# Kernel tuning notes

Measured on AMD Instinct MI355X. Metric: run time of the kernel, lower is better.

Reference implementation:

```python
import jax, jax.numpy as jnp
import numpy as np

HIDDEN = 1024
HEADS = 16
DK = HIDDEN // HEADS  # 64
B, N = 2, 2048


def setup_inputs() -> dict:
    key = jax.random.key(0)
    ks = jax.random.split(key, 12)
    s = 0.02
    return {
        "q": jax.random.normal(ks[0], (B, N, HIDDEN), jnp.float32),
        "k": jax.random.normal(ks[1], (B, N, HIDDEN), jnp.float32),
        "v": jax.random.normal(ks[2], (B, N, HIDDEN), jnp.float32),
        "attn_bias": jax.random.normal(ks[3], (B, N, N), jnp.float32),
        "attention_mask": jnp.zeros((B, N, N), jnp.float32),
        # projection weights stored [in, out]
        "Wq": jax.random.normal(ks[4], (HIDDEN, HIDDEN), jnp.float32) * s,
        "bq": jnp.zeros((HIDDEN,), jnp.float32),
        "Wk": jax.random.normal(ks[5], (HIDDEN, HIDDEN), jnp.float32) * s,
        "bk": jnp.zeros((HIDDEN,), jnp.float32),
        "Wv": jax.random.normal(ks[6], (HIDDEN, HIDDEN), jnp.float32) * s,
        "bv": jnp.zeros((HIDDEN,), jnp.float32),
        "Wo": jax.random.normal(ks[7], (HIDDEN, HIDDEN), jnp.float32) * s,
        "bo": jnp.zeros((HIDDEN,), jnp.float32),
    }


def reference(q, k, v, attn_bias, attention_mask, Wq, bq, Wk, bk, Wv, bv, Wo, bo):
    b, n, _ = q.shape
    scale = DK ** (-0.5)
    # project and split heads: [B, H, N, Dk]
    qh = (q @ Wq + bq).reshape(b, n, HEADS, DK).transpose(0, 2, 1, 3)
    kh = (k @ Wk + bk).reshape(b, -1, HEADS, DK).transpose(0, 2, 1, 3)
    vh = (v @ Wv + bv).reshape(b, -1, HEADS, DK).transpose(0, 2, 1, 3)
    # scaled scores + additive bias/mask broadcast over heads: [B, H, N, N]
    scores = jnp.einsum('bhnd,bhmd->bhnm', qh * scale, kh)
    scores = scores + attn_bias[:, None, :, :] + attention_mask[:, None, :, :]
    probs = jax.nn.softmax(scores, axis=-1)  # dropout is identity at inference
    ctx = jnp.einsum('bhnm,bhmd->bhnd', probs, vh)
    ctx = ctx.transpose(0, 2, 1, 3).reshape(b, n, HEADS * DK)
    return ctx @ Wo + bo
```

## Files before the change

kernel.cpp:

```cpp
#include <hip/hip_runtime.h>
#include <hip/hip_bf16.h>

#define HIDDEN 1024
#define NHEADS 16
#define DKH   64
#define BATCH 2
#define SEQ   2048
#define MTOT  (BATCH*SEQ)

using bf16x8 = __attribute__((ext_vector_type(8))) short;
using f32x4  = __attribute__((ext_vector_type(4))) float;
using u16x4  = __attribute__((ext_vector_type(4))) unsigned short;

__device__ __forceinline__ unsigned short f2bf(float f) {
    union { __hip_bfloat16 h; unsigned short u; } v;
    v.h = __float2bfloat16(f);
    return v.u;
}

__device__ __forceinline__ float asfloat(unsigned int u) {
    union { unsigned int u; float f; } v; v.u = u; return v.f;
}

__device__ __forceinline__ float fexp2(float x) {
#if __has_builtin(__builtin_amdgcn_exp2f)
    return __builtin_amdgcn_exp2f(x);
#else
    return exp2f(x);
#endif
}

__device__ __forceinline__ void gload16(const unsigned short* g, unsigned short* l) {
    __builtin_amdgcn_global_load_lds((const __attribute__((address_space(1))) void*)g,
                                     (__attribute__((address_space(3))) void*)l, 16, 0, 0);
}

#define L2E 1.44269504088896340736f

__global__ __launch_bounds__(256) void prep(const float4* __restrict__ q,
                                            const float4* __restrict__ k,
                                            const float4* __restrict__ v,
                                            u16x4* __restrict__ qkv_bf,
                                            const float* __restrict__ Wq,
                                            const float* __restrict__ Wk,
                                            const float* __restrict__ Wv,
                                            const float* __restrict__ Wo,
                                            unsigned short* __restrict__ wt,
                                            const float* __restrict__ bias,
                                            const float* __restrict__ mask,
                                            unsigned short* __restrict__ biasf) {
    __shared__ __align__(16) char sh[16640];
    float (*tile)[65] = (float (*)[65])sh;
    unsigned short (*lb)[520] = (unsigned short (*)[520])sh;
    const int bid = blockIdx.x, t = threadIdx.x;
    if (bid < 12288) {
        int i = bid * 256 + t;
        const int per = MTOT * HIDDEN / 4;
        const float4* src; int tt;
        if (i < per)            { src = q; tt = 0; }
        else if (i < 2 * per)   { src = k; tt = 1; }
        else                    { src = v; tt = 2; }
        float4 f = src[i - tt * per];
        u16x4 o; o.x = f2bf(f.x); o.y = f2bf(f.y); o.z = f2bf(f.z); o.w = f2bf(f.w);
        qkv_bf[i] = o;
    } else if (bid < 13312) {
        int r = bid - 12288;
        const int z = r >> 8; r &= 255;
        const int kb = (r >> 4) * 64, nb = (r & 15) * 64;
        const float* W = (z == 0) ? Wq : (z == 1) ? Wk : (z == 2) ? Wv : Wo;
        unsigned short* out = wt + (size_t)z * HIDDEN * HIDDEN;
        #pragma unroll
        for (int i = 0; i < 16; i++) {
            int idx = i * 256 + t; int rr = idx >> 6, c = idx & 63;
            tile[rr][c] = W[(size_t)(kb + rr) * HIDDEN + nb + c];
        }
        __syncthreads();
        #pragma unroll
        for (int i = 0; i < 16; i++) {
            int idx = i * 256 + t; int n = idx >> 6, kk = idx & 63;
            out[(size_t)(nb + n) * HIDDEN + kb + kk] = f2bf(tile[kk][n]);
        }
    } else {
        const int cb = bid - 13312;
        const int chunk = cb & 3, g = (cb >> 2) & 127, b = cb >> 9;
        const float* bp = bias + ((size_t)b * SEQ + g * 16) * SEQ + chunk * 512;
        const float* mp = mask + ((size_t)b * SEQ + g * 16) * SEQ + chunk * 512;
        #pragma unroll
        for (int i = 0; i < 8; i++) {
            int idx = i * 256 + t;
            int row = idx >> 7, c4 = (idx & 127) * 4;
            float4 bv4 = *(const float4*)(bp + (size_t)row * SEQ + c4);
            float4 mv4 = *(const float4*)(mp + (size_t)row * SEQ + c4);
            union { u16x4 v; unsigned short s[4]; } o;
            o.s[0] = f2bf((bv4.x + mv4.x) * L2E);
            o.s[1] = f2bf((bv4.y + mv4.y) * L2E);
            o.s[2] = f2bf((bv4.z + mv4.z) * L2E);
            o.s[3] = f2bf((bv4.w + mv4.w) * L2E);
            *(u16x4*)&lb[row][c4] = o.v;
        }
        __syncthreads();
        const int w = t >> 6, ln = t & 63;
        const int quad = ln >> 4, c16 = ln & 15;
        unsigned short* ob = biasf + (((size_t)b * 128 + g) * 64 + chunk * 16) * 512 + ln * 8;
        #pragma unroll
        for (int it = 0; it < 4; it++) {
            int ttl = it * 4 + w;
            *(bf16x8*)(ob + (size_t)ttl * 512) = *(const bf16x8*)&lb[c16][ttl * 32 + quad * 8];
        }
    }
}

__device__ __forceinline__ void gemm_core_128(const unsigned short* __restrict__ X,
                                              const unsigned short* __restrict__ Wt,
                                              unsigned short* smem,
                                              int mbase, int nbase, f32x4 acc[4][4]) {
    const int tid = threadIdx.x, w = tid >> 6, ln = tid & 63;
    const int qr = (w >> 1) * 64, qc = (w & 1) * 64;
    const int g = ln >> 4, c16 = ln & 15;
    #pragma unroll
    for (int rt = 0; rt < 4; rt++)
        #pragma unroll
        for (int ct = 0; ct < 4; ct++) acc[rt][ct] = (f32x4){0.f, 0.f, 0.f, 0.f};

    for (int kk = 0; kk < HIDDEN; kk += 64) {
        __syncthreads();
        #pragma unroll
        for (int pass = 0; pass < 4; pass++) {
            int L = pass * 256 + tid;
            int r = L >> 3, c = (L & 7) ^ (r & 7);
            gload16(X  + (size_t)(mbase + r) * HIDDEN + kk + c * 8,
                    smem + (size_t)(pass * 256 + w * 64) * 8);
            gload16(Wt + (size_t)(nbase + r) * HIDDEN + kk + c * 8,
                    smem + 8192 + (size_t)(pass * 256 + w * 64) * 8);
        }
        __syncthreads();
        #pragma unroll
        for (int ks = 0; ks < 2; ks++) {
            bf16x8 af[4], bfr[4];
            #pragma unroll
            for (int rt = 0; rt < 4; rt++) {
                int r = qr + rt * 16 + c16;
                int ch = (g + ks * 4) ^ (r & 7);
                af[rt] = *(const bf16x8*)(smem + (size_t)(r * 8 + ch) * 8);
            }
            #pragma unroll
            for (int ct = 0; ct < 4; ct++) {
                int n = qc + ct * 16 + c16;
                int ch = (g + ks * 4) ^ (n & 7);
                bfr[ct] = *(const bf16x8*)(smem + 8192 + (size_t)(n * 8 + ch) * 8);
            }
            #pragma unroll
            for (int rt = 0; rt < 4; rt++)
                #pragma unroll
                for (int ct = 0; ct < 4; ct++)
                    acc[rt][ct] = __builtin_amdgcn_mfma_f32_16x16x32_bf16(af[rt], bfr[ct], acc[rt][ct], 0, 0, 0);
        }
    }
    __syncthreads();
}

__global__ __launch_bounds__(256, 2) void proj_gemm(const unsigned short* __restrict__ Xall,
                                                    const unsigned short* __restrict__ Wtall,
                                                    const float* __restrict__ bq,
                                                    const float* __restrict__ bk,
                                                    const float* __restrict__ bv,
                                                    unsigned short* __restrict__ qh,
                                                    unsigned short* __restrict__ khs,
                                                    unsigned short* __restrict__ vts) {
    __shared__ __align__(16) unsigned short smem[18432];
    const int z = blockIdx.z;
    const unsigned short* X  = Xall  + (size_t)z * MTOT * HIDDEN;
    const unsigned short* Wt = Wtall + (size_t)z * HIDDEN * HIDDEN;
    const float* bias = (z == 0) ? bq : (z == 1) ? bk : bv;
    const int mbase = blockIdx.x * 128, nbase = blockIdx.y * 128;
    const int tid = threadIdx.x, w = tid >> 6, ln = tid & 63;
    const int qr = (w >> 1) * 64, qc = (w & 1) * 64;
    const int g = ln >> 4, c16 = ln & 15;

    f32x4 acc[4][4];
    gemm_core_128(X, Wt, smem, mbase, nbase, acc);

    const float scale = (z == 0) ? (0.125f * L2E) : 1.0f;
    float bias_v[4];
    #pragma unroll
    for (int ct = 0; ct < 4; ct++) bias_v[ct] = bias[nbase + qc + ct * 16 + c16];

    unsigned short* eld = smem + w * 4608;
    #pragma unroll
    for (int rt = 0; rt < 4; rt++)
        #pragma unroll
        for (int ct = 0; ct < 4; ct++)
            #pragma unroll
            for (int r4 = 0; r4 < 4; r4++) {
                int row_l = rt * 16 + g * 4 + r4;
                int col_l = ct * 16 + c16;
                float val = (acc[rt][ct][r4] + bias_v[ct]) * scale;
                if (z == 2) eld[col_l * 72 + row_l] = f2bf(val);
                else        eld[row_l * 72 + col_l] = f2bf(val);
            }
    __syncthreads();

    const int b = mbase >> 11;
    const int pos0 = (mbase & 2047) + qr;
    const int h = (nbase + qc) >> 6;
    const int bh = b * NHEADS + h;
    if (z == 0) {
        const int row8 = ln >> 3, col8 = (ln & 7) * 8;
        unsigned short* dst0 = qh + ((size_t)bh * SEQ + pos0) * DKH;
        #pragma unroll
        for (int j = 0; j < 8; j++) {
            int row = j * 8 + row8;
            *(bf16x8*)(dst0 + row * 64 + col8) = *(const bf16x8*)&eld[row * 72 + col8];
        }
    } else if (z == 1) {
        unsigned short* base = khs + ((size_t)bh * 64 + (pos0 >> 5)) * 2048;
        const int kvp = (c16 >> 2) * 8 + (c16 & 3);
        #pragma unroll
        for (int j = 0; j < 8; j++) {
            int tloc = j >> 2, ks = (j >> 1) & 1, kvs = j & 1;
            int kvl = tloc * 32 + kvp + kvs * 4;
            *(bf16x8*)(base + tloc * 2048 + ks * 1024 + kvs * 512 + ln * 8)
                = *(const bf16x8*)&eld[kvl * 72 + ks * 32 + g * 8];
        }
    } else {
        unsigned short* base = vts + ((size_t)bh * 64 + (pos0 >> 5)) * 2048;
        #pragma unroll
        for (int j = 0; j < 8; j++) {
            int tloc = j >> 2, dt = j & 3;
            *(bf16x8*)(base + tloc * 2048 + dt * 512 + ln * 8)
                = *(const bf16x8*)&eld[(dt * 16 + c16) * 72 + tloc * 32 + g * 8];
        }
    }
}

__global__ __launch_bounds__(256, 2) void attn(const unsigned short* __restrict__ qh,
                                               const unsigned short* __restrict__ khs,
                                               const unsigned short* __restrict__ vts,
                                               const unsigned short* __restrict__ biasf,
                                               unsigned short* __restrict__ ctx) {
    __shared__ __align__(16) unsigned short smem[16384];
    const int tid = threadIdx.x, w = tid >> 6, ln = tid & 63;
    const int quad = ln >> 4, c16 = ln & 15;
    const int bid = blockIdx.x;
    const int xcd = bid & 7, jj = bid >> 3;
    const int bh = xcd * 4 + (jj >> 4);
    const int qb = jj & 15;
    const int b = bh >> 4, h = bh & 15;

    bf16x8 qf[2][2];
    #pragma unroll
    for (int qsub = 0; qsub < 2; qsub++) {
        const unsigned short* qp = qh + ((size_t)bh * SEQ + qb * 128 + w * 32 + qsub * 16 + c16) * DKH + quad * 8;
        qf[qsub][0] = *(const bf16x8*)qp;
        qf[qsub][1] = *(const bf16x8*)(qp + 32);
    }

    const unsigned short* kT = khs + (size_t)bh * 131072;
    const unsigned short* vT = vts + (size_t)bh * 131072;
    const unsigned short* bb0 = biasf + (((size_t)b * 128 + qb * 8 + w * 2) * 64) * 512 + ln * 8;
    const unsigned short* bb1 = bb0 + 32768;

    f32x4 accv[4][2];
    #pragma unroll
    for (int dt = 0; dt < 4; dt++)
        #pragma unroll
        for (int qsub = 0; qsub < 2; qsub++) accv[dt][qsub] = (f32x4){0.f, 0.f, 0.f, 0.f};
    float lacc[2] = {0.f, 0.f};

    bf16x8 bcur[2][4];
    #pragma unroll
    for (int j = 0; j < 4; j++) {
        bcur[0][j] = *(const bf16x8*)(bb0 + j * 512);
        bcur[1][j] = *(const bf16x8*)(bb1 + j * 512);
    }

    for (int T = 0; T < 16; T++) {
        __syncthreads();
        {
            const unsigned short* ksrc = kT + T * 8192 + w * 512 + ln * 8;
            const unsigned short* vsrc = vT + T * 8192 + w * 512 + ln * 8;
            unsigned short* lk = smem + w * 512;
            unsigned short* lv = smem + 8192 + w * 512;
            #pragma unroll
            for (int p = 0; p < 4; p++) {
                gload16(ksrc + p * 2048, lk + p * 2048);
                gload16(vsrc + p * 2048, lv + p * 2048);
            }
        }
        bf16x8 bnext[2][4];
        {
            const int Tn = (T < 15) ? T + 1 : 15;
            #pragma unroll
            for (int j = 0; j < 4; j++) {
                bnext[0][j] = *(const bf16x8*)(bb0 + (Tn * 4 + j) * 512);
                bnext[1][j] = *(const bf16x8*)(bb1 + (Tn * 4 + j) * 512);
            }
        }
        __syncthreads();
        #pragma unroll
        for (int j = 0; j < 4; j++) {
            bf16x8 kf00 = *(const bf16x8*)(smem + j * 2048 + ln * 8);
            bf16x8 kf01 = *(const bf16x8*)(smem + j * 2048 + 512 + ln * 8);
            bf16x8 kf10 = *(const bf16x8*)(smem + j * 2048 + 1024 + ln * 8);
            bf16x8 kf11 = *(const bf16x8*)(smem + j * 2048 + 1536 + ln * 8);
            bf16x8 vf[4];
            #pragma unroll
            for (int dt = 0; dt < 4; dt++)
                vf[dt] = *(const bf16x8*)(smem + 8192 + j * 2048 + dt * 512 + ln * 8);
            #pragma unroll
            for (int qsub = 0; qsub < 2; qsub++) {
                const unsigned int* bd = (const unsigned int*)&bcur[qsub][j];
                f32x4 s0, s1;
                s0[0] = asfloat(bd[0] << 16); s0[1] = asfloat(bd[0] & 0xFFFF0000u);
                s0[2] = asfloat(bd[1] << 16); s0[3] = asfloat(bd[1] & 0xFFFF0000u);
                s1[0] = asfloat(bd[2] << 16); s1[1] = asfloat(bd[2] & 0xFFFF0000u);
                s1[2] = asfloat(bd[3] << 16); s1[3] = asfloat(bd[3] & 0xFFFF0000u);
                s0 = __builtin_amdgcn_mfma_f32_16x16x32_bf16(kf00, qf[qsub][0], s0, 0, 0, 0);
                s0 = __builtin_amdgcn_mfma_f32_16x16x32_bf16(kf10, qf[qsub][1], s0, 0, 0, 0);
                s1 = __builtin_amdgcn_mfma_f32_16x16x32_bf16(kf01, qf[qsub][0], s1, 0, 0, 0);
                s1 = __builtin_amdgcn_mfma_f32_16x16x32_bf16(kf11, qf[qsub][1], s1, 0, 0, 0);
                #pragma unroll
                for (int r = 0; r < 4; r++) { s0[r] = fexp2(s0[r]); s1[r] = fexp2(s1[r]); }
                lacc[qsub] += ((s0[0] + s0[1]) + (s0[2] + s0[3]))
                            + ((s1[0] + s1[1]) + (s1[2] + s1[3]));
                union { bf16x8 v; __hip_bfloat162 hh[4]; } pu;
                pu.hh[0] = __float22bfloat162_rn(make_float2(s0[0], s0[1]));
                pu.hh[1] = __float22bfloat162_rn(make_float2(s0[2], s0[3]));
                pu.hh[2] = __float22bfloat162_rn(make_float2(s1[0], s1[1]));
                pu.hh[3] = __float22bfloat162_rn(make_float2(s1[2], s1[3]));
                #pragma unroll
                for (int dt = 0; dt < 4; dt++)
                    accv[dt][qsub] = __builtin_amdgcn_mfma_f32_16x16x32_bf16(vf[dt], pu.v, accv[dt][qsub], 0, 0, 0);
            }
            bcur[0][j] = bnext[0][j];
            bcur[1][j] = bnext[1][j];
        }
    }

    float inv[2];
    #pragma unroll
    for (int qsub = 0; qsub < 2; qsub++) {
        float l = lacc[qsub];
        l += __shfl_xor(l, 16);
        l += __shfl_xor(l, 32);
        inv[qsub] = 1.0f / l;
    }
    __syncthreads();
    unsigned short* ot = smem + w * 2304;
    #pragma unroll
    for (int dt = 0; dt < 4; dt++)
        #pragma unroll
        for (int qsub = 0; qsub < 2; qsub++)
            #pragma unroll
            for (int r = 0; r < 4; r += 2) {
                union { __hip_bfloat162 hh; unsigned int u; } pk;
                pk.hh = __float22bfloat162_rn(make_float2(accv[dt][qsub][r] * inv[qsub],
                                                         accv[dt][qsub][r + 1] * inv[qsub]));
                *(unsigned int*)&ot[(qsub * 16 + c16) * 72 + dt * 16 + quad * 4 + r] = pk.u;
            }
    const int qrow2 = ln >> 1, half = ln & 1;
    const unsigned short* srcp = ot + qrow2 * 72 + half * 32;
    unsigned short* dstp = ctx + ((size_t)b * SEQ + qb * 128 + w * 32 + qrow2) * HIDDEN
                         + h * 64 + half * 32;
    #pragma unroll
    for (int kk = 0; kk < 4; kk++)
        *(bf16x8*)(dstp + kk * 8) = *(const bf16x8*)(srcp + kk * 8);
}

__global__ __launch_bounds__(256, 2) void outproj(const unsigned short* __restrict__ X,
                                                  const unsigned short* __restrict__ Wt,
                                                  const float* __restrict__ bo,
                                                  float* __restrict__ out) {
    __shared__ __align__(16) unsigned short smem[16384];
    const int mbase = blockIdx.x * 128, nbase = blockIdx.y * 128;
    const int tid = threadIdx.x, w = tid >> 6, ln = tid & 63;
    const int qr = (w >> 1) * 64, qc = (w & 1) * 64;
    const int g = ln >> 4, c16 = ln & 15;

    f32x4 acc[4][4];
    gemm_core_128(X, Wt, smem, mbase, nbase, acc);

    float bo_v[4];
    #pragma unroll
    for (int ct = 0; ct < 4; ct++) bo_v[ct] = bo[nbase + qc + ct * 16 + c16];
    #pragma unroll
    for (int rt = 0; rt < 4; rt++)
        #pragma unroll
        for (int ct = 0; ct < 4; ct++)
            #pragma unroll
            for (int r4 = 0; r4 < 4; r4++)
                out[(size_t)(mbase + qr + rt * 16 + g * 4 + r4) * HIDDEN + nbase + qc + ct * 16 + c16]
                    = acc[rt][ct][r4] + bo_v[ct];
}

extern "C" void kernel_launch(void* const* d_in, const int* in_sizes, int n_in,
                              void* d_out, int out_size, void* d_ws, size_t ws_size,
                              hipStream_t stream) {
    const float* q    = (const float*)d_in[0];
    const float* k    = (const float*)d_in[1];
    const float* v    = (const float*)d_in[2];
    const float* bias = (const float*)d_in[3];
    const float* mask = (const float*)d_in[4];
    const float* Wq   = (const float*)d_in[5];
    const float* bq   = (const float*)d_in[6];
    const float* Wk   = (const float*)d_in[7];
    const float* bk   = (const float*)d_in[8];
    const float* Wv   = (const float*)d_in[9];
    const float* bv   = (const float*)d_in[10];
    const float* Wo   = (const float*)d_in[11];
    const float* bo   = (const float*)d_in[12];

    char* ws = (char*)d_ws;
    unsigned short* qkv_bf = (unsigned short*)(ws);
    unsigned short* wt     = (unsigned short*)(ws + 25165824);
    unsigned short* qh     = (unsigned short*)(ws + 33554432);
    unsigned short* khs    = (unsigned short*)(ws + 41943040);
    unsigned short* vts    = (unsigned short*)(ws + 50331648);
    unsigned short* ctx    = (unsigned short*)(ws + 58720256);
    unsigned short* biasf  = (unsigned short*)(ws + 67108864);

    prep<<<14336, 256, 0, stream>>>((const float4*)q, (const float4*)k, (const float4*)v,
                                    (u16x4*)qkv_bf, Wq, Wk, Wv, Wo, wt, bias, mask, biasf);
    proj_gemm<<<dim3(32, 8, 3), 256, 0, stream>>>(qkv_bf, wt, bq, bk, bv, qh, khs, vts);
    attn<<<512, 256, 0, stream>>>(qh, khs, vts, biasf, ctx);
    outproj<<<dim3(32, 8), 256, 0, stream>>>(ctx, wt + (size_t)3 * HIDDEN * HIDDEN, bo,
                                             (float*)d_out);
}
```

Before: 270.3 us.

## Halve attention query tile to 64 rows and double block count

Each attention block now handles 64 query rows instead of 128, with every wave covering 16 rows instead of 32. The grid grows from 512 to 1024 blocks and launch bounds allow four blocks per CU, so register use per thread drops and more waves are resident to hide latency. In exchange, every K/V tile staged in LDS is reused by half as many queries, which doubles the global and LDS traffic for K and V.

New measurement: 280.1 us. 3.6% more time.

```diff
diff --git a/kernel.cpp b/kernel.cpp
--- a/kernel.cpp
+++ b/kernel.cpp
@@ -233,7 +233,7 @@
     }
 }
 
-__global__ __launch_bounds__(256, 2) void attn(const unsigned short* __restrict__ qh,
+__global__ __launch_bounds__(256, 4) void attn(const unsigned short* __restrict__ qh,
                                                const unsigned short* __restrict__ khs,
                                                const unsigned short* __restrict__ vts,
                                                const unsigned short* __restrict__ biasf,
@@ -243,36 +243,29 @@
     const int quad = ln >> 4, c16 = ln & 15;
     const int bid = blockIdx.x;
     const int xcd = bid & 7, jj = bid >> 3;
-    const int bh = xcd * 4 + (jj >> 4);
-    const int qb = jj & 15;
+    const int bh = xcd * 4 + (jj >> 5);
+    const int qb = jj & 31;
     const int b = bh >> 4, h = bh & 15;
 
-    bf16x8 qf[2][2];
-    #pragma unroll
-    for (int qsub = 0; qsub < 2; qsub++) {
-        const unsigned short* qp = qh + ((size_t)bh * SEQ + qb * 128 + w * 32 + qsub * 16 + c16) * DKH + quad * 8;
-        qf[qsub][0] = *(const bf16x8*)qp;
-        qf[qsub][1] = *(const bf16x8*)(qp + 32);
+    bf16x8 qf[2];
+    {
+        const unsigned short* qp = qh + ((size_t)bh * SEQ + qb * 64 + w * 16 + c16) * DKH + quad * 8;
+        qf[0] = *(const bf16x8*)qp;
+        qf[1] = *(const bf16x8*)(qp + 32);
     }
 
     const unsigned short* kT = khs + (size_t)bh * 131072;
     const unsigned short* vT = vts + (size_t)bh * 131072;
-    const unsigned short* bb0 = biasf + (((size_t)b * 128 + qb * 8 + w * 2) * 64) * 512 + ln * 8;
-    const unsigned short* bb1 = bb0 + 32768;
-
-    f32x4 accv[4][2];
-    #pragma unroll
-    for (int dt = 0; dt < 4; dt++)
-        #pragma unroll
-        for (int qsub = 0; qsub < 2; qsub++) accv[dt][qsub] = (f32x4){0.f, 0.f, 0.f, 0.f};
-    float lacc[2] = {0.f, 0.f};
-
-    bf16x8 bcur[2][4];
-    #pragma unroll
-    for (int j = 0; j < 4; j++) {
-        bcur[0][j] = *(const bf16x8*)(bb0 + j * 512);
-        bcur[1][j] = *(const bf16x8*)(bb1 + j * 512);
-    }
+    const unsigned short* bb = biasf + (((size_t)b * 128 + qb * 4 + w) * 64) * 512 + ln * 8;
+
+    f32x4 accv[4];
+    #pragma unroll
+    for (int dt = 0; dt < 4; dt++) accv[dt] = (f32x4){0.f, 0.f, 0.f, 0.f};
+    float lacc = 0.f;
+
+    bf16x8 bcur[4];
+    #pragma unroll
+    for (int j = 0; j < 4; j++) bcur[j] = *(const bf16x8*)(bb + j * 512);
 
     for (int T = 0; T < 16; T++) {
         __syncthreads();
@@ -287,14 +280,12 @@
                 gload16(vsrc + p * 2048, lv + p * 2048);
             }
         }
-        bf16x8 bnext[2][4];
+        bf16x8 bnext[4];
         {
             const int Tn = (T < 15) ? T + 1 : 15;
             #pragma unroll
-            for (int j = 0; j < 4; j++) {
-                bnext[0][j] = *(const bf16x8*)(bb0 + (Tn * 4 + j) * 512);
-                bnext[1][j] = *(const bf16x8*)(bb1 + (Tn * 4 + j) * 512);
-            }
+            for (int j = 0; j < 4; j++)
+                bnext[j] = *(const bf16x8*)(bb + (Tn * 4 + j) * 512);
         }
         __syncthreads();
         #pragma unroll
@@ -307,64 +298,53 @@
             #pragma unroll
             for (int dt = 0; dt < 4; dt++)
                 vf[dt] = *(const bf16x8*)(smem + 8192 + j * 2048 + dt * 512 + ln * 8);
-            #pragma unroll
-            for (int qsub = 0; qsub < 2; qsub++) {
-                const unsigned int* bd = (const unsigned int*)&bcur[qsub][j];
-                f32x4 s0, s1;
-                s0[0] = asfloat(bd[0] << 16); s0[1] = asfloat(bd[0] & 0xFFFF0000u);
-                s0[2] = asfloat(bd[1] << 16); s0[3] = asfloat(bd[1] & 0xFFFF0000u);
-                s1[0] = asfloat(bd[2] << 16); s1[1] = asfloat(bd[2] & 0xFFFF0000u);
-                s1[2] = asfloat(bd[3] << 16); s1[3] = asfloat(bd[3] & 0xFFFF0000u);
-                s0 = __builtin_amdgcn_mfma_f32_16x16x32_bf16(kf00, qf[qsub][0], s0, 0, 0, 0);
-                s0 = __builtin_amdgcn_mfma_f32_16x16x32_bf16(kf10, qf[qsub][1], s0, 0, 0, 0);
-                s1 = __builtin_amdgcn_mfma_f32_16x16x32_bf16(kf01, qf[qsub][0], s1, 0, 0, 0);
-                s1 = __builtin_amdgcn_mfma_f32_16x16x32_bf16(kf11, qf[qsub][1], s1, 0, 0, 0);
-                #pragma unroll
-                for (int r = 0; r < 4; r++) { s0[r] = fexp2(s0[r]); s1[r] = fexp2(s1[r]); }
-                lacc[qsub] += ((s0[0] + s0[1]) + (s0[2] + s0[3]))
-                            + ((s1[0] + s1[1]) + (s1[2] + s1[3]));
-                union { bf16x8 v; __hip_bfloat162 hh[4]; } pu;
-                pu.hh[0] = __float22bfloat162_rn(make_float2(s0[0], s0[1]));
-                pu.hh[1] = __float22bfloat162_rn(make_float2(s0[2], s0[3]));
-                pu.hh[2] = __float22bfloat162_rn(make_float2(s1[0], s1[1]));
-                pu.hh[3] = __float22bfloat162_rn(make_float2(s1[2], s1[3]));
-                #pragma unroll
-                for (int dt = 0; dt < 4; dt++)
-                    accv[dt][qsub] = __builtin_amdgcn_mfma_f32_16x16x32_bf16(vf[dt], pu.v, accv[dt][qsub], 0, 0, 0);
-            }
-            bcur[0][j] = bnext[0][j];
-            bcur[1][j] = bnext[1][j];
+            const unsigned int* bd = (const unsigned int*)&bcur[j];
+            f32x4 s0, s1;
+            s0[0] = asfloat(bd[0] << 16); s0[1] = asfloat(bd[0] & 0xFFFF0000u);
+            s0[2] = asfloat(bd[1] << 16); s0[3] = asfloat(bd[1] & 0xFFFF0000u);
+            s1[0] = asfloat(bd[2] << 16); s1[1] = asfloat(bd[2] & 0xFFFF0000u);
+            s1[2] = asfloat(bd[3] << 16); s1[3] = asfloat(bd[3] & 0xFFFF0000u);
+            s0 = __builtin_amdgcn_mfma_f32_16x16x32_bf16(kf00, qf[0], s0, 0, 0, 0);
+            s0 = __builtin_amdgcn_mfma_f32_16x16x32_bf16(kf10, qf[1], s0, 0, 0, 0);
+            s1 = __builtin_amdgcn_mfma_f32_16x16x32_bf16(kf01, qf[0], s1, 0, 0, 0);
+            s1 = __builtin_amdgcn_mfma_f32_16x16x32_bf16(kf11, qf[1], s1, 0, 0, 0);
+            #pragma unroll
+            for (int r = 0; r < 4; r++) { s0[r] = fexp2(s0[r]); s1[r] = fexp2(s1[r]); }
+            lacc += ((s0[0] + s0[1]) + (s0[2] + s0[3]))
+                  + ((s1[0] + s1[1]) + (s1[2] + s1[3]));
+            union { bf16x8 v; __hip_bfloat162 hh[4]; } pu;
+            pu.hh[0] = __float22bfloat162_rn(make_float2(s0[0], s0[1]));
+            pu.hh[1] = __float22bfloat162_rn(make_float2(s0[2], s0[3]));
+            pu.hh[2] = __float22bfloat162_rn(make_float2(s1[0], s1[1]));
+            pu.hh[3] = __float22bfloat162_rn(make_float2(s1[2], s1[3]));
+            #pragma unroll
+            for (int dt = 0; dt < 4; dt++)
+                accv[dt] = __builtin_amdgcn_mfma_f32_16x16x32_bf16(vf[dt], pu.v, accv[dt], 0, 0, 0);
+            bcur[j] = bnext[j];
         }
     }
 
-    float inv[2];
-    #pragma unroll
-    for (int qsub = 0; qsub < 2; qsub++) {
-        float l = lacc[qsub];
-        l += __shfl_xor(l, 16);
-        l += __shfl_xor(l, 32);
-        inv[qsub] = 1.0f / l;
-    }
+    float l = lacc;
+    l += __shfl_xor(l, 16);
+    l += __shfl_xor(l, 32);
+    const float inv = 1.0f / l;
     __syncthreads();
-    unsigned short* ot = smem + w * 2304;
+    unsigned short* ot = smem + w * 1152;
     #pragma unroll
     for (int dt = 0; dt < 4; dt++)
         #pragma unroll
-        for (int qsub = 0; qsub < 2; qsub++)
-            #pragma unroll
-            for (int r = 0; r < 4; r += 2) {
-                union { __hip_bfloat162 hh; unsigned int u; } pk;
-                pk.hh = __float22bfloat162_rn(make_float2(accv[dt][qsub][r] * inv[qsub],
-                                                         accv[dt][qsub][r + 1] * inv[qsub]));
-                *(unsigned int*)&ot[(qsub * 16 + c16) * 72 + dt * 16 + quad * 4 + r] = pk.u;
-            }
-    const int qrow2 = ln >> 1, half = ln & 1;
-    const unsigned short* srcp = ot + qrow2 * 72 + half * 32;
-    unsigned short* dstp = ctx + ((size_t)b * SEQ + qb * 128 + w * 32 + qrow2) * HIDDEN
-                         + h * 64 + half * 32;
-    #pragma unroll
-    for (int kk = 0; kk < 4; kk++)
-        *(bf16x8*)(dstp + kk * 8) = *(const bf16x8*)(srcp + kk * 8);
+        for (int r = 0; r < 4; r += 2) {
+            union { __hip_bfloat162 hh; unsigned int u; } pk;
+            pk.hh = __float22bfloat162_rn(make_float2(accv[dt][r] * inv,
+                                                     accv[dt][r + 1] * inv));
+            *(unsigned int*)&ot[c16 * 72 + dt * 16 + quad * 4 + r] = pk.u;
+        }
+    const int row = ln >> 2, seg = ln & 3;
+    const unsigned short* srcp = ot + row * 72 + seg * 16;
+    unsigned short* dstp = ctx + ((size_t)b * SEQ + qb * 64 + w * 16 + row) * HIDDEN
+                         + h * 64 + seg * 16;
+    *(bf16x8*)(dstp)     = *(const bf16x8*)(srcp);
+    *(bf16x8*)(dstp + 8) = *(const bf16x8*)(srcp + 8);
 }
 
 __global__ __launch_bounds__(256, 2) void outproj(const unsigned short* __restrict__ X,
@@ -422,7 +402,7 @@
     prep<<<14336, 256, 0, stream>>>((const float4*)q, (const float4*)k, (const float4*)v,
                                     (u16x4*)qkv_bf, Wq, Wk, Wv, Wo, wt, bias, mask, biasf);
     proj_gemm<<<dim3(32, 8, 3), 256, 0, stream>>>(qkv_bf, wt, bq, bk, bv, qh, khs, vts);
-    attn<<<512, 256, 0, stream>>>(qh, khs, vts, biasf, ctx);
+    attn<<<1024, 256, 0, stream>>>(qh, khs, vts, biasf, ctx);
     outproj<<<dim3(32, 8), 256, 0, stream>>>(ctx, wt + (size_t)3 * HIDDEN * HIDDEN, bo,
                                              (float*)d_out);
 }
```
